# Optimization experiments

Measured on AMD Instinct MI355X. Metric: run time of the kernel, lower is better.

The kernel has to match this reference:

```python
import jax, jax.numpy as jnp
import numpy as np

N_NODES = 50000


def _gcn_layer(x, src, dst, W, b, n_nodes):
    """DGL GraphConv with norm='both', bias, ReLU activation."""
    ones = jnp.ones(src.shape[0], dtype=x.dtype)
    deg_out = jax.ops.segment_sum(ones, src, num_segments=n_nodes)
    deg_in = jax.ops.segment_sum(ones, dst, num_segments=n_nodes)
    deg_out = jnp.clip(deg_out, 1.0, None)
    deg_in = jnp.clip(deg_in, 1.0, None)
    h = x * jax.lax.rsqrt(deg_out)[:, None]          # src-side normalization
    m = jax.ops.segment_sum(h[src], dst, num_segments=n_nodes)  # SpMM gather/scatter
    m = m * jax.lax.rsqrt(deg_in)[:, None]           # dst-side normalization
    return jax.nn.relu(m @ W + b)


def setup_inputs() -> dict:
    key = jax.random.key(0)
    ks = jax.random.split(key, 8)
    N, E, ES, D = N_NODES, 800000, 200000, 128
    x = jax.random.normal(ks[0], (N, D), dtype=jnp.float32)
    edge_src = jax.random.randint(ks[1], (E,), 0, N)
    edge_dst = jax.random.randint(ks[2], (E,), 0, N)
    score_src = jax.random.randint(ks[3], (ES,), 0, N)
    score_dst = jax.random.randint(ks[4], (ES,), 0, N)
    W1 = jax.random.normal(ks[5], (D, D), dtype=jnp.float32) / np.sqrt(D)
    W2 = jax.random.normal(ks[6], (D, D), dtype=jnp.float32) / np.sqrt(D)
    b1 = jnp.zeros((D,), dtype=jnp.float32)
    b2 = jnp.zeros((D,), dtype=jnp.float32)
    return {"x": x, "edge_src": edge_src, "edge_dst": edge_dst,
            "score_src": score_src, "score_dst": score_dst,
            "W1": W1, "b1": b1, "W2": W2, "b2": b2}


def reference(x, edge_src, edge_dst, score_src, score_dst, W1, b1, W2, b2):
    n = x.shape[0]
    h = _gcn_layer(x, edge_src, edge_dst, W1, b1, n)
    h = _gcn_layer(h, edge_src, edge_dst, W2, b2, n)
    # edge-wise u_dot_v scoring -> [E_score, 1]
    score = jnp.sum(h[score_src] * h[score_dst], axis=-1, keepdims=True)
    return score
```

## Files before the change

### kernel.cpp

```cpp
#include <hip/hip_runtime.h>

#define D 128

__global__ void zero_u32(unsigned* p, int n) {
  int i = blockIdx.x * blockDim.x + threadIdx.x;
  int stride = gridDim.x * blockDim.x;
  for (; i < n; i += stride) p[i] = 0u;
}

__global__ void count_deg(const int* __restrict__ src, const int* __restrict__ dst,
                          unsigned* cnt_out, unsigned* cnt_in, int E) {
  int e = blockIdx.x * blockDim.x + threadIdx.x;
  if (e < E) {
    atomicAdd(&cnt_out[src[e]], 1u);
    atomicAdd(&cnt_in[dst[e]], 1u);
  }
}

__global__ void make_rsqrt(const unsigned* __restrict__ cnt_out,
                           const unsigned* __restrict__ cnt_in,
                           float* __restrict__ rs_out, float* __restrict__ rs_in, int N) {
  int i = blockIdx.x * blockDim.x + threadIdx.x;
  if (i < N) {
    float vo = (float)cnt_out[i]; if (vo < 1.f) vo = 1.f;
    float vi = (float)cnt_in[i];  if (vi < 1.f) vi = 1.f;
    rs_out[i] = rsqrtf(vo);
    rs_in[i]  = rsqrtf(vi);
  }
}

__global__ void prescale_rows(const float* __restrict__ x, const float* __restrict__ rs,
                              float* __restrict__ xp, int total4) {
  int i = blockIdx.x * blockDim.x + threadIdx.x;
  if (i < total4) {
    int n = i >> 5;
    float r = rs[n];
    float4 v = ((const float4*)x)[i];
    v.x *= r; v.y *= r; v.z *= r; v.w *= r;
    ((float4*)xp)[i] = v;
  }
}

__global__ void scan_p1(const unsigned* __restrict__ cnt, int n,
                        int* __restrict__ excl, int* __restrict__ bsum) {
  __shared__ int s[256];
  int t = threadIdx.x;
  int i = blockIdx.x * 256 + t;
  int v = (i < n) ? (int)cnt[i] : 0;
  s[t] = v;
  __syncthreads();
  for (int off = 1; off < 256; off <<= 1) {
    int add = (t >= off) ? s[t - off] : 0;
    __syncthreads();
    s[t] += add;
    __syncthreads();
  }
  if (i < n) excl[i] = s[t] - v;
  if (t == 255) bsum[blockIdx.x] = s[255];
}

__global__ void scan_p2(int* bsum, int nb) {
  __shared__ int s[256];
  int t = threadIdx.x;
  int v = (t < nb) ? bsum[t] : 0;
  s[t] = v;
  __syncthreads();
  for (int off = 1; off < 256; off <<= 1) {
    int add = (t >= off) ? s[t - off] : 0;
    __syncthreads();
    s[t] += add;
    __syncthreads();
  }
  if (t < nb) bsum[t] = s[t] - v;
}

__global__ void scan_p3(int* __restrict__ row_ptr, int* __restrict__ cursor,
                        const int* __restrict__ bsum, int n, int E) {
  int i = blockIdx.x * blockDim.x + threadIdx.x;
  if (i < n) {
    int e = row_ptr[i] + bsum[i >> 8];
    row_ptr[i] = e;
    cursor[i]  = e;
  }
  if (i == 0) row_ptr[n] = E;
}

__global__ void fill_csr(const int* __restrict__ src, const int* __restrict__ dst,
                         int* cursor, int* __restrict__ csr_src, int E) {
  int e = blockIdx.x * blockDim.x + threadIdx.x;
  if (e < E) {
    int d = dst[e];
    int pos = atomicAdd(&cursor[d], 1);
    csr_src[pos] = src[e];
  }
}

__global__ __launch_bounds__(256) void spmm(const float* __restrict__ X,
    const int* __restrict__ row_ptr, const int* __restrict__ csr_src,
    const float* __restrict__ rs_in, float* __restrict__ out, int N) {
  int n = blockIdx.x * 4 + (threadIdx.x >> 6);
  int lane = threadIdx.x & 63;
  if (n >= N) return;
  int beg = row_ptr[n], end = row_ptr[n + 1];
  float r = rs_in[n];
  const float2* X2 = (const float2*)X;
  float ax = 0.f, ay = 0.f;
  int e = beg;
  for (; e + 4 <= end; e += 4) {
    int s0 = csr_src[e];
    int s1 = csr_src[e + 1];
    int s2 = csr_src[e + 2];
    int s3 = csr_src[e + 3];
    float2 v0 = X2[(size_t)s0 * 64 + lane];
    float2 v1 = X2[(size_t)s1 * 64 + lane];
    float2 v2 = X2[(size_t)s2 * 64 + lane];
    float2 v3 = X2[(size_t)s3 * 64 + lane];
    ax += (v0.x + v1.x) + (v2.x + v3.x);
    ay += (v0.y + v1.y) + (v2.y + v3.y);
  }
  for (; e < end; ++e) {
    int s = csr_src[e];
    float2 v = X2[(size_t)s * 64 + lane];
    ax += v.x;
    ay += v.y;
  }
  float2 o;
  o.x = ax * r;
  o.y = ay * r;
  ((float2*)out)[(size_t)n * 64 + lane] = o;
}

__global__ __launch_bounds__(256) void gemm_bias_relu(
    const float* __restrict__ M, const float* __restrict__ W,
    const float* __restrict__ bias, const float* __restrict__ postscale,
    float* __restrict__ out, int nrows) {
  __shared__ float Wl[D * D];
  int t = threadIdx.x;
  {
    const float4* W4 = (const float4*)W;
    float4* Wl4 = (float4*)Wl;
#pragma unroll
    for (int i = 0; i < 16; ++i) Wl4[t + i * 256] = W4[t + i * 256];
  }
  __syncthreads();

  int tx = t & 15;
  int ty = t >> 4;
  int rbase = blockIdx.x * 64 + ty * 4;
  int c0 = tx * 8;

  float acc[4][8];
#pragma unroll
  for (int i = 0; i < 4; ++i)
#pragma unroll
    for (int c = 0; c < 8; ++c) acc[i][c] = 0.f;

  int r[4];
#pragma unroll
  for (int i = 0; i < 4; ++i) {
    r[i] = rbase + i;
    if (r[i] > nrows - 1) r[i] = nrows - 1;
  }

  const float4* M4 = (const float4*)M;
  for (int k4 = 0; k4 < D / 4; ++k4) {
    float4 mv[4];
#pragma unroll
    for (int i = 0; i < 4; ++i) mv[i] = M4[r[i] * (D / 4) + k4];
    float mk[4][4];
#pragma unroll
    for (int i = 0; i < 4; ++i) {
      mk[i][0] = mv[i].x; mk[i][1] = mv[i].y; mk[i][2] = mv[i].z; mk[i][3] = mv[i].w;
    }
#pragma unroll
    for (int kk = 0; kk < 4; ++kk) {
      const float* wrow = Wl + (k4 * 4 + kk) * D + c0;
      float4 w0 = *(const float4*)(wrow);
      float4 w1 = *(const float4*)(wrow + 4);
      float wv[8] = {w0.x, w0.y, w0.z, w0.w, w1.x, w1.y, w1.z, w1.w};
#pragma unroll
      for (int i = 0; i < 4; ++i)
#pragma unroll
        for (int c = 0; c < 8; ++c) acc[i][c] += mk[i][kk] * wv[c];
    }
  }

  __syncthreads();

#pragma unroll
  for (int i = 0; i < 4; ++i) {
    int rr = rbase + i;
    if (rr < nrows) {
      float ps = postscale ? postscale[rr] : 1.f;
      float4 o0, o1;
      o0.x = fmaxf(acc[i][0] + bias[c0 + 0], 0.f) * ps;
      o0.y = fmaxf(acc[i][1] + bias[c0 + 1], 0.f) * ps;
      o0.z = fmaxf(acc[i][2] + bias[c0 + 2], 0.f) * ps;
      o0.w = fmaxf(acc[i][3] + bias[c0 + 3], 0.f) * ps;
      o1.x = fmaxf(acc[i][4] + bias[c0 + 4], 0.f) * ps;
      o1.y = fmaxf(acc[i][5] + bias[c0 + 5], 0.f) * ps;
      o1.z = fmaxf(acc[i][6] + bias[c0 + 6], 0.f) * ps;
      o1.w = fmaxf(acc[i][7] + bias[c0 + 7], 0.f) * ps;
      *(float4*)(out + rr * D + c0)     = o0;
      *(float4*)(out + rr * D + c0 + 4) = o1;
    }
  }
}

__global__ void score_kernel(const float* __restrict__ H, const int* __restrict__ ss,
                             const int* __restrict__ sd, float* __restrict__ out, int ES) {
  int wid = (int)((blockIdx.x * blockDim.x + threadIdx.x) >> 6);
  int lane = threadIdx.x & 63;
  if (wid >= ES) return;
  int a = ss[wid], b = sd[wid];
  const float* pa = H + (size_t)a * D;
  const float* pb = H + (size_t)b * D;
  float p = pa[lane] * pb[lane] + pa[lane + 64] * pb[lane + 64];
#pragma unroll
  for (int off = 32; off > 0; off >>= 1) p += __shfl_xor(p, off, 64);
  if (lane == 0) out[wid] = p;
}

extern "C" void kernel_launch(void* const* d_in, const int* in_sizes, int n_in,
                              void* d_out, int out_size, void* d_ws, size_t ws_size,
                              hipStream_t stream) {
  const float* x   = (const float*)d_in[0];
  const int* esrc  = (const int*)d_in[1];
  const int* edst  = (const int*)d_in[2];
  const int* ssrc  = (const int*)d_in[3];
  const int* sdst  = (const int*)d_in[4];
  const float* W1  = (const float*)d_in[5];
  const float* b1  = (const float*)d_in[6];
  const float* W2  = (const float*)d_in[7];
  const float* b2  = (const float*)d_in[8];
  float* out = (float*)d_out;

  const int N  = in_sizes[0] / D;
  const int E  = in_sizes[1];
  const int ES = in_sizes[3];

  char* w = (char*)d_ws;
  auto take = [&](size_t bytes) {
    char* p = w;
    w += (bytes + 255) & ~(size_t)255;
    return p;
  };
  unsigned* cnt     = (unsigned*)take((size_t)2 * N * 4);
  unsigned* cnt_out = cnt;
  unsigned* cnt_in  = cnt + N;
  float* rs_out = (float*)take((size_t)N * 4);
  float* rs_in  = (float*)take((size_t)N * 4);
  int* row_ptr  = (int*)take((size_t)(N + 1) * 4);
  int* cursor   = (int*)take((size_t)N * 4);
  int* bsum     = (int*)take(256 * 4);
  int* csr_src  = (int*)take((size_t)E * 4);
  float* bufA   = (float*)take((size_t)N * D * 4);
  float* bufB   = (float*)take((size_t)N * D * 4);

  int nb = (N + 255) / 256;

  zero_u32<<<(2 * N + 255) / 256, 256, 0, stream>>>(cnt, 2 * N);
  count_deg<<<(E + 255) / 256, 256, 0, stream>>>(esrc, edst, cnt_out, cnt_in, E);
  make_rsqrt<<<(N + 255) / 256, 256, 0, stream>>>(cnt_out, cnt_in, rs_out, rs_in, N);
  scan_p1<<<nb, 256, 0, stream>>>(cnt_in, N, row_ptr, bsum);
  scan_p2<<<1, 256, 0, stream>>>(bsum, nb);
  scan_p3<<<nb, 256, 0, stream>>>(row_ptr, cursor, bsum, N, E);
  fill_csr<<<(E + 255) / 256, 256, 0, stream>>>(esrc, edst, cursor, csr_src, E);

  prescale_rows<<<(N * 32 + 255) / 256, 256, 0, stream>>>(x, rs_out, bufB, N * 32);

  spmm<<<(N + 3) / 4, 256, 0, stream>>>(bufB, row_ptr, csr_src, rs_in, bufA, N);
  gemm_bias_relu<<<(N + 63) / 64, 256, 0, stream>>>(bufA, W1, b1, rs_out, bufA, N);

  spmm<<<(N + 3) / 4, 256, 0, stream>>>(bufA, row_ptr, csr_src, rs_in, bufB, N);
  gemm_bias_relu<<<(N + 63) / 64, 256, 0, stream>>>(bufB, W2, b2, nullptr, bufB, N);

  score_kernel<<<(ES + 3) / 4, 256, 0, stream>>>(bufB, ssrc, sdst, out, ES);
}
```

Before: 425.0 us.

## Replicate degree counters and CSR cursors across blocks to spread atomics

Degree counting and CSR filling now use R=8 replicated counter and cursor arrays selected by block index, so atomics on hot nodes are spread over separate addresses. A reduction kernel sums the replicas into rsqrt norms and total in-degree, and a new kernel computes per-replica cursor bases from the row pointer. The replicas live in bufA scratch before it is reused. This adds an extra kernel and more zeroing and reduction traffic. With random edges contention is already low, so the benefit may be limited.

```diff
diff --git a/kernel.cpp b/kernel.cpp
--- a/kernel.cpp
+++ b/kernel.cpp
@@ -1,6 +1,7 @@
 #include <hip/hip_runtime.h>
 
 #define D 128
+#define R 8
 
 __global__ void zero_u32(unsigned* p, int n) {
   int i = blockIdx.x * blockDim.x + threadIdx.x;
@@ -8,36 +9,32 @@
   for (; i < n; i += stride) p[i] = 0u;
 }
 
-__global__ void count_deg(const int* __restrict__ src, const int* __restrict__ dst,
-                          unsigned* cnt_out, unsigned* cnt_in, int E) {
+__global__ void count_deg_rep(const int* __restrict__ src, const int* __restrict__ dst,
+                              unsigned* __restrict__ rep, int E, int N) {
   int e = blockIdx.x * blockDim.x + threadIdx.x;
+  unsigned roff = (unsigned)(blockIdx.x & (R - 1)) * 2u * (unsigned)N;
   if (e < E) {
-    atomicAdd(&cnt_out[src[e]], 1u);
-    atomicAdd(&cnt_in[dst[e]], 1u);
-  }
-}
-
-__global__ void make_rsqrt(const unsigned* __restrict__ cnt_out,
-                           const unsigned* __restrict__ cnt_in,
-                           float* __restrict__ rs_out, float* __restrict__ rs_in, int N) {
+    atomicAdd(&rep[roff + src[e]], 1u);
+    atomicAdd(&rep[roff + (unsigned)N + dst[e]], 1u);
+  }
+}
+
+__global__ void make_rsqrt_rep(const unsigned* __restrict__ rep,
+                               float* __restrict__ rs_out, float* __restrict__ rs_in,
+                               unsigned* __restrict__ cnt_in_total, int N) {
   int i = blockIdx.x * blockDim.x + threadIdx.x;
   if (i < N) {
-    float vo = (float)cnt_out[i]; if (vo < 1.f) vo = 1.f;
-    float vi = (float)cnt_in[i];  if (vi < 1.f) vi = 1.f;
-    rs_out[i] = rsqrtf(vo);
-    rs_in[i]  = rsqrtf(vi);
-  }
-}
-
-__global__ void prescale_rows(const float* __restrict__ x, const float* __restrict__ rs,
-                              float* __restrict__ xp, int total4) {
-  int i = blockIdx.x * blockDim.x + threadIdx.x;
-  if (i < total4) {
-    int n = i >> 5;
-    float r = rs[n];
-    float4 v = ((const float4*)x)[i];
-    v.x *= r; v.y *= r; v.z *= r; v.w *= r;
-    ((float4*)xp)[i] = v;
+    unsigned vo = 0, vi = 0;
+#pragma unroll
+    for (int r = 0; r < R; ++r) {
+      vo += rep[(size_t)r * 2 * N + i];
+      vi += rep[(size_t)r * 2 * N + N + i];
+    }
+    cnt_in_total[i] = vi;
+    float fo = vo ? (float)vo : 1.f;
+    float fi = vi ? (float)vi : 1.f;
+    rs_out[i] = rsqrtf(fo);
+    rs_in[i]  = rsqrtf(fi);
   }
 }
 
@@ -74,24 +71,46 @@
   if (t < nb) bsum[t] = s[t] - v;
 }
 
-__global__ void scan_p3(int* __restrict__ row_ptr, int* __restrict__ cursor,
-                        const int* __restrict__ bsum, int n, int E) {
-  int i = blockIdx.x * blockDim.x + threadIdx.x;
-  if (i < n) {
-    int e = row_ptr[i] + bsum[i >> 8];
-    row_ptr[i] = e;
-    cursor[i]  = e;
-  }
+__global__ void scan_p3(int* __restrict__ row_ptr, const int* __restrict__ bsum,
+                        int n, int E) {
+  int i = blockIdx.x * blockDim.x + threadIdx.x;
+  if (i < n) row_ptr[i] += bsum[i >> 8];
   if (i == 0) row_ptr[n] = E;
 }
 
-__global__ void fill_csr(const int* __restrict__ src, const int* __restrict__ dst,
-                         int* cursor, int* __restrict__ csr_src, int E) {
+__global__ void make_cursors(const int* __restrict__ row_ptr,
+                             const unsigned* __restrict__ rep,
+                             int* __restrict__ cursor, int N) {
+  int i = blockIdx.x * blockDim.x + threadIdx.x;
+  if (i < N) {
+    int base = row_ptr[i];
+#pragma unroll
+    for (int r = 0; r < R; ++r) {
+      cursor[(size_t)r * N + i] = base;
+      base += (int)rep[(size_t)r * 2 * N + N + i];
+    }
+  }
+}
+
+__global__ void fill_csr_rep(const int* __restrict__ src, const int* __restrict__ dst,
+                             int* cursor, int* __restrict__ csr_src, int E, int N) {
   int e = blockIdx.x * blockDim.x + threadIdx.x;
   if (e < E) {
     int d = dst[e];
-    int pos = atomicAdd(&cursor[d], 1);
+    int pos = atomicAdd(&cursor[(size_t)(blockIdx.x & (R - 1)) * N + d], 1);
     csr_src[pos] = src[e];
+  }
+}
+
+__global__ void prescale_rows(const float* __restrict__ x, const float* __restrict__ rs,
+                              float* __restrict__ xp, int total4) {
+  int i = blockIdx.x * blockDim.x + threadIdx.x;
+  if (i < total4) {
+    int n = i >> 5;
+    float r = rs[n];
+    float4 v = ((const float4*)x)[i];
+    v.x *= r; v.y *= r; v.z *= r; v.w *= r;
+    ((float4*)xp)[i] = v;
   }
 }
 
@@ -245,27 +264,29 @@
     w += (bytes + 255) & ~(size_t)255;
     return p;
   };
-  unsigned* cnt     = (unsigned*)take((size_t)2 * N * 4);
-  unsigned* cnt_out = cnt;
-  unsigned* cnt_in  = cnt + N;
   float* rs_out = (float*)take((size_t)N * 4);
   float* rs_in  = (float*)take((size_t)N * 4);
+  unsigned* cnt_in_total = (unsigned*)take((size_t)N * 4);
   int* row_ptr  = (int*)take((size_t)(N + 1) * 4);
-  int* cursor   = (int*)take((size_t)N * 4);
   int* bsum     = (int*)take(256 * 4);
   int* csr_src  = (int*)take((size_t)E * 4);
   float* bufA   = (float*)take((size_t)N * D * 4);
   float* bufB   = (float*)take((size_t)N * D * 4);
 
-  int nb = (N + 255) / 256;
-
-  zero_u32<<<(2 * N + 255) / 256, 256, 0, stream>>>(cnt, 2 * N);
-  count_deg<<<(E + 255) / 256, 256, 0, stream>>>(esrc, edst, cnt_out, cnt_in, E);
-  make_rsqrt<<<(N + 255) / 256, 256, 0, stream>>>(cnt_out, cnt_in, rs_out, rs_in, N);
-  scan_p1<<<nb, 256, 0, stream>>>(cnt_in, N, row_ptr, bsum);
+  unsigned* rep = (unsigned*)bufA;
+  int* cursor   = (int*)(bufA + (size_t)2 * N * R);
+
+  int nb  = (N + 255) / 256;
+  int ngE = (E + 255) / 256;
+
+  zero_u32<<<2048, 256, 0, stream>>>(rep, 2 * N * R);
+  count_deg_rep<<<ngE, 256, 0, stream>>>(esrc, edst, rep, E, N);
+  make_rsqrt_rep<<<nb, 256, 0, stream>>>(rep, rs_out, rs_in, cnt_in_total, N);
+  scan_p1<<<nb, 256, 0, stream>>>(cnt_in_total, N, row_ptr, bsum);
   scan_p2<<<1, 256, 0, stream>>>(bsum, nb);
-  scan_p3<<<nb, 256, 0, stream>>>(row_ptr, cursor, bsum, N, E);
-  fill_csr<<<(E + 255) / 256, 256, 0, stream>>>(esrc, edst, cursor, csr_src, E);
+  scan_p3<<<nb, 256, 0, stream>>>(row_ptr, bsum, N, E);
+  make_cursors<<<nb, 256, 0, stream>>>(row_ptr, rep, cursor, N);
+  fill_csr_rep<<<ngE, 256, 0, stream>>>(esrc, edst, cursor, csr_src, E, N);
 
   prescale_rows<<<(N * 32 + 255) / 256, 256, 0, stream>>>(x, rs_out, bufB, N * 32);
 
```

After: 431.7 us. About the same (+1.6%).

## Replace atomic degree count and CSR fill with two-level bucketed binning

Applied to the files above, without the earlier changes.

Degree counting, prefix scan and CSR construction are replaced with a two-level radix-style binning. Edges are first histogrammed into 64-node buckets using shared-memory atomics, then a single-block scan runs, then edges are scattered into bucket regions. A per-bucket pass finally builds row_ptr, csr_src and both rsqrt degree vectors locally. This replaces many contended global atomics and several launches, but the binning kernels use only 64 blocks, which may underuse the GPU, and bufA is reused as scratch.

```diff
diff --git a/kernel.cpp b/kernel.cpp
--- a/kernel.cpp
+++ b/kernel.cpp
@@ -1,6 +1,8 @@
 #include <hip/hip_runtime.h>
 
 #define D 128
+#define NBLK_BIN 64
+#define MAXBUCK 1024
 
 __global__ void zero_u32(unsigned* p, int n) {
   int i = blockIdx.x * blockDim.x + threadIdx.x;
@@ -8,24 +10,130 @@
   for (; i < n; i += stride) p[i] = 0u;
 }
 
-__global__ void count_deg(const int* __restrict__ src, const int* __restrict__ dst,
-                          unsigned* cnt_out, unsigned* cnt_in, int E) {
-  int e = blockIdx.x * blockDim.x + threadIdx.x;
-  if (e < E) {
-    atomicAdd(&cnt_out[src[e]], 1u);
-    atomicAdd(&cnt_in[dst[e]], 1u);
-  }
-}
-
-__global__ void make_rsqrt(const unsigned* __restrict__ cnt_out,
-                           const unsigned* __restrict__ cnt_in,
-                           float* __restrict__ rs_out, float* __restrict__ rs_in, int N) {
-  int i = blockIdx.x * blockDim.x + threadIdx.x;
-  if (i < N) {
-    float vo = (float)cnt_out[i]; if (vo < 1.f) vo = 1.f;
-    float vi = (float)cnt_in[i];  if (vi < 1.f) vi = 1.f;
-    rs_out[i] = rsqrtf(vo);
-    rs_in[i]  = rsqrtf(vi);
+__global__ __launch_bounds__(256) void phaseA(const int* __restrict__ src,
+    const int* __restrict__ dst, unsigned* __restrict__ gcnt_dst,
+    unsigned* __restrict__ gcnt_src, int E, int NBUCK, int chunk) {
+  __shared__ unsigned hd[MAXBUCK], hs[MAXBUCK];
+  int t = threadIdx.x;
+  for (int j = t; j < NBUCK; j += 256) { hd[j] = 0u; hs[j] = 0u; }
+  __syncthreads();
+  int beg = blockIdx.x * chunk, end = min(E, beg + chunk);
+  for (int i = beg + t; i < end; i += 256) {
+    atomicAdd(&hd[dst[i] >> 6], 1u);
+    atomicAdd(&hs[src[i] >> 6], 1u);
+  }
+  __syncthreads();
+  for (int j = t; j < NBUCK; j += 256) {
+    if (hd[j]) atomicAdd(&gcnt_dst[j], hd[j]);
+    if (hs[j]) atomicAdd(&gcnt_src[j], hs[j]);
+  }
+}
+
+__global__ __launch_bounds__(1024) void phaseB(const unsigned* __restrict__ gcnt_dst,
+    const unsigned* __restrict__ gcnt_src, int* __restrict__ base_dst,
+    int* __restrict__ base_src, int* __restrict__ gcur_dst,
+    int* __restrict__ gcur_src, int* __restrict__ row_ptr,
+    int N, int E, int NBUCK) {
+  __shared__ int s[1024];
+  int t = threadIdx.x;
+  int v = (t < NBUCK) ? (int)gcnt_dst[t] : 0;
+  s[t] = v;
+  __syncthreads();
+  for (int off = 1; off < 1024; off <<= 1) {
+    int a = (t >= off) ? s[t - off] : 0;
+    __syncthreads(); s[t] += a; __syncthreads();
+  }
+  if (t < NBUCK) { int e = s[t] - v; base_dst[t] = e; gcur_dst[t] = e; }
+  if (t == 0) { base_dst[NBUCK] = E; row_ptr[N] = E; }
+  __syncthreads();
+  v = (t < NBUCK) ? (int)gcnt_src[t] : 0;
+  s[t] = v;
+  __syncthreads();
+  for (int off = 1; off < 1024; off <<= 1) {
+    int a = (t >= off) ? s[t - off] : 0;
+    __syncthreads(); s[t] += a; __syncthreads();
+  }
+  if (t < NBUCK) { int e = s[t] - v; base_src[t] = e; gcur_src[t] = e; }
+  if (t == 0) base_src[NBUCK] = E;
+}
+
+__global__ __launch_bounds__(256) void phaseC(const int* __restrict__ src,
+    const int* __restrict__ dst, int* gcur_dst, int* gcur_src,
+    unsigned long long* __restrict__ bkt, int* __restrict__ bkt_src,
+    int E, int NBUCK, int chunk) {
+  __shared__ int hd[MAXBUCK], hs[MAXBUCK];
+  int t = threadIdx.x;
+  for (int j = t; j < NBUCK; j += 256) { hd[j] = 0; hs[j] = 0; }
+  __syncthreads();
+  int beg = blockIdx.x * chunk, end = min(E, beg + chunk);
+  for (int i = beg + t; i < end; i += 256) {
+    atomicAdd(&hd[dst[i] >> 6], 1);
+    atomicAdd(&hs[src[i] >> 6], 1);
+  }
+  __syncthreads();
+  for (int j = t; j < NBUCK; j += 256) {
+    int c = hd[j]; if (c) hd[j] = atomicAdd(&gcur_dst[j], c);
+    c = hs[j];     if (c) hs[j] = atomicAdd(&gcur_src[j], c);
+  }
+  __syncthreads();
+  for (int i = beg + t; i < end; i += 256) {
+    int d = dst[i], s2 = src[i];
+    int p = atomicAdd(&hd[d >> 6], 1);
+    bkt[p] = ((unsigned long long)(unsigned)s2 << 32) | (unsigned)d;
+    int q = atomicAdd(&hs[s2 >> 6], 1);
+    bkt_src[q] = s2;
+  }
+}
+
+__global__ __launch_bounds__(256) void phaseD_dst(
+    const unsigned long long* __restrict__ bkt, const int* __restrict__ base_dst,
+    int* __restrict__ row_ptr, float* __restrict__ rs_in,
+    int* __restrict__ csr_src, int N) {
+  __shared__ int hist[64], excl[65], cur[64];
+  int b = blockIdx.x, t = threadIdx.x;
+  int beg = base_dst[b], end = base_dst[b + 1];
+  if (t < 64) hist[t] = 0;
+  __syncthreads();
+  for (int i = beg + t; i < end; i += 256)
+    atomicAdd(&hist[(int)(bkt[i] & 0xffffffffu) & 63], 1);
+  __syncthreads();
+  if (t == 0) {
+    int acc = 0;
+    for (int j = 0; j < 64; ++j) { excl[j] = acc; acc += hist[j]; }
+    excl[64] = acc;
+  }
+  __syncthreads();
+  if (t < 64) {
+    cur[t] = excl[t];
+    int v = b * 64 + t;
+    if (v < N) {
+      row_ptr[v] = beg + excl[t];
+      rs_in[v] = rsqrtf((float)(hist[t] > 0 ? hist[t] : 1));
+    }
+  }
+  __syncthreads();
+  for (int i = beg + t; i < end; i += 256) {
+    unsigned long long p = bkt[i];
+    int d = (int)(p & 0xffffffffu);
+    int pos = atomicAdd(&cur[d & 63], 1);
+    csr_src[beg + pos] = (int)(p >> 32);
+  }
+}
+
+__global__ __launch_bounds__(256) void phaseD_src(
+    const int* __restrict__ bkt_src, const int* __restrict__ base_src,
+    float* __restrict__ rs_out, int N) {
+  __shared__ int hist[64];
+  int b = blockIdx.x, t = threadIdx.x;
+  int beg = base_src[b], end = base_src[b + 1];
+  if (t < 64) hist[t] = 0;
+  __syncthreads();
+  for (int i = beg + t; i < end; i += 256)
+    atomicAdd(&hist[bkt_src[i] & 63], 1);
+  __syncthreads();
+  if (t < 64) {
+    int v = b * 64 + t;
+    if (v < N) rs_out[v] = rsqrtf((float)(hist[t] > 0 ? hist[t] : 1));
   }
 }
 
@@ -38,60 +146,6 @@
     float4 v = ((const float4*)x)[i];
     v.x *= r; v.y *= r; v.z *= r; v.w *= r;
     ((float4*)xp)[i] = v;
-  }
-}
-
-__global__ void scan_p1(const unsigned* __restrict__ cnt, int n,
-                        int* __restrict__ excl, int* __restrict__ bsum) {
-  __shared__ int s[256];
-  int t = threadIdx.x;
-  int i = blockIdx.x * 256 + t;
-  int v = (i < n) ? (int)cnt[i] : 0;
-  s[t] = v;
-  __syncthreads();
-  for (int off = 1; off < 256; off <<= 1) {
-    int add = (t >= off) ? s[t - off] : 0;
-    __syncthreads();
-    s[t] += add;
-    __syncthreads();
-  }
-  if (i < n) excl[i] = s[t] - v;
-  if (t == 255) bsum[blockIdx.x] = s[255];
-}
-
-__global__ void scan_p2(int* bsum, int nb) {
-  __shared__ int s[256];
-  int t = threadIdx.x;
-  int v = (t < nb) ? bsum[t] : 0;
-  s[t] = v;
-  __syncthreads();
-  for (int off = 1; off < 256; off <<= 1) {
-    int add = (t >= off) ? s[t - off] : 0;
-    __syncthreads();
-    s[t] += add;
-    __syncthreads();
-  }
-  if (t < nb) bsum[t] = s[t] - v;
-}
-
-__global__ void scan_p3(int* __restrict__ row_ptr, int* __restrict__ cursor,
-                        const int* __restrict__ bsum, int n, int E) {
-  int i = blockIdx.x * blockDim.x + threadIdx.x;
-  if (i < n) {
-    int e = row_ptr[i] + bsum[i >> 8];
-    row_ptr[i] = e;
-    cursor[i]  = e;
-  }
-  if (i == 0) row_ptr[n] = E;
-}
-
-__global__ void fill_csr(const int* __restrict__ src, const int* __restrict__ dst,
-                         int* cursor, int* __restrict__ csr_src, int E) {
-  int e = blockIdx.x * blockDim.x + threadIdx.x;
-  if (e < E) {
-    int d = dst[e];
-    int pos = atomicAdd(&cursor[d], 1);
-    csr_src[pos] = src[e];
   }
 }
 
@@ -238,6 +292,7 @@
   const int N  = in_sizes[0] / D;
   const int E  = in_sizes[1];
   const int ES = in_sizes[3];
+  const int NBUCK = (N + 63) >> 6;
 
   char* w = (char*)d_ws;
   auto take = [&](size_t bytes) {
@@ -245,27 +300,33 @@
     w += (bytes + 255) & ~(size_t)255;
     return p;
   };
-  unsigned* cnt     = (unsigned*)take((size_t)2 * N * 4);
-  unsigned* cnt_out = cnt;
-  unsigned* cnt_in  = cnt + N;
   float* rs_out = (float*)take((size_t)N * 4);
   float* rs_in  = (float*)take((size_t)N * 4);
   int* row_ptr  = (int*)take((size_t)(N + 1) * 4);
-  int* cursor   = (int*)take((size_t)N * 4);
-  int* bsum     = (int*)take(256 * 4);
+  unsigned* gcnt = (unsigned*)take((size_t)2 * MAXBUCK * 4);
+  int* base_dst = (int*)take((size_t)(MAXBUCK + 1) * 4);
+  int* base_src = (int*)take((size_t)(MAXBUCK + 1) * 4);
+  int* gcur_dst = (int*)take((size_t)MAXBUCK * 4);
+  int* gcur_src = (int*)take((size_t)MAXBUCK * 4);
   int* csr_src  = (int*)take((size_t)E * 4);
   float* bufA   = (float*)take((size_t)N * D * 4);
   float* bufB   = (float*)take((size_t)N * D * 4);
 
-  int nb = (N + 255) / 256;
-
-  zero_u32<<<(2 * N + 255) / 256, 256, 0, stream>>>(cnt, 2 * N);
-  count_deg<<<(E + 255) / 256, 256, 0, stream>>>(esrc, edst, cnt_out, cnt_in, E);
-  make_rsqrt<<<(N + 255) / 256, 256, 0, stream>>>(cnt_out, cnt_in, rs_out, rs_in, N);
-  scan_p1<<<nb, 256, 0, stream>>>(cnt_in, N, row_ptr, bsum);
-  scan_p2<<<1, 256, 0, stream>>>(bsum, nb);
-  scan_p3<<<nb, 256, 0, stream>>>(row_ptr, cursor, bsum, N, E);
-  fill_csr<<<(E + 255) / 256, 256, 0, stream>>>(esrc, edst, cursor, csr_src, E);
+  unsigned* gcnt_dst = gcnt;
+  unsigned* gcnt_src = gcnt + MAXBUCK;
+  unsigned long long* bkt = (unsigned long long*)bufA;
+  int* bkt_src = (int*)(bufA + (size_t)E * 2);
+
+  const int chunk = (E + NBLK_BIN - 1) / NBLK_BIN;
+
+  zero_u32<<<8, 256, 0, stream>>>(gcnt, 2 * MAXBUCK);
+  phaseA<<<NBLK_BIN, 256, 0, stream>>>(esrc, edst, gcnt_dst, gcnt_src, E, NBUCK, chunk);
+  phaseB<<<1, 1024, 0, stream>>>(gcnt_dst, gcnt_src, base_dst, base_src,
+                                 gcur_dst, gcur_src, row_ptr, N, E, NBUCK);
+  phaseC<<<NBLK_BIN, 256, 0, stream>>>(esrc, edst, gcur_dst, gcur_src,
+                                       bkt, bkt_src, E, NBUCK, chunk);
+  phaseD_dst<<<NBUCK, 256, 0, stream>>>(bkt, base_dst, row_ptr, rs_in, csr_src, N);
+  phaseD_src<<<NBUCK, 256, 0, stream>>>(bkt_src, base_src, rs_out, N);
 
   prescale_rows<<<(N * 32 + 255) / 256, 256, 0, stream>>>(x, rs_out, bufB, N * 32);
 
```

Measured after the change: 382.6 us. 10.0% less time.
